# Optimization experiments

Hardware: AMD Instinct MI355X
Metric: run time of the kernel (lower is better)

## Reference

```python
import jax, jax.numpy as jnp
import numpy as np

B, N, C = 8, 4096, 1024
H = 16
D = C // H  # head_dim = 64
SCALE = D ** -0.5


def setup_inputs() -> dict:
    key = jax.random.key(0)
    ks = jax.random.split(key, 5)
    std = C ** -0.5
    return {
        "x": jax.random.normal(ks[0], (B, N, C), dtype=jnp.float32),
        "Wq": jax.random.normal(ks[1], (C, C), dtype=jnp.float32) * std,
        "Wk": jax.random.normal(ks[2], (C, C), dtype=jnp.float32) * std,
        "Wv": jax.random.normal(ks[3], (C, C), dtype=jnp.float32) * std,
        "Wo": jax.random.normal(ks[4], (C, C), dtype=jnp.float32) * std,
        "bo": jnp.zeros((C,), dtype=jnp.float32),
    }


def reference(x, Wq, Wk, Wv, Wo, bo):
    b, n, c = x.shape
    # projections -> (B, N, H, D)
    q = (x @ Wq).reshape(b, n, H, D)
    k = (x @ Wk).reshape(b, n, H, D)
    v = (x @ Wv).reshape(b, n, H, D)
    # feature maps: softmax over head_dim for q, over sequence for k
    q = jax.nn.softmax(q, axis=-1) * SCALE
    k = jax.nn.softmax(k, axis=1)
    # O(N) linear attention: kv summary then apply to q
    kv = jnp.einsum("bnhf,bnhd->bhfd", k, v)   # (B, H, D, D)
    y = jnp.einsum("bnhf,bhfd->bnhd", q, kv)   # (B, N, H, D)
    y = y.reshape(b, n, H * D)
    return y @ Wo + bo
```

## Files before the change

### kernel.cpp

```cpp
#include <hip/hip_runtime.h>


typedef unsigned short u16;
typedef __bf16 bf16x8v __attribute__((ext_vector_type(8)));
typedef float f32x4 __attribute__((ext_vector_type(4)));
typedef u16 u16x8 __attribute__((ext_vector_type(8)));
typedef u16 u16x4 __attribute__((ext_vector_type(4)));

#define AS1C(p) (const __attribute__((address_space(1))) void*)(p)
#define AS3(p)  (__attribute__((address_space(3))) void*)(p)

__device__ __forceinline__ float b2f(u16 u) {
    union { unsigned u; float f; } c; c.u = ((unsigned)u) << 16; return c.f;
}
__device__ __forceinline__ u16 f2b(float f) {
    union { float f; unsigned u; } c; c.f = f;
    unsigned x = c.u + 0x7fffu + ((c.u >> 16) & 1u);
    return (u16)(x >> 16);
}

__global__ void cast_x_kernel(const float* __restrict__ in, u16* __restrict__ out, long n4) {
    long i = (long)blockIdx.x * blockDim.x + threadIdx.x;
    long stride = (long)gridDim.x * blockDim.x;
    for (long j = i; j < n4; j += stride) {
        float4 v = ((const float4*)in)[j];
        u16x4 o = { f2b(v.x), f2b(v.y), f2b(v.z), f2b(v.w) };
        ((u16x4*)out)[j] = o;
    }
}

__global__ void transpose_cast(const float* __restrict__ src, u16* __restrict__ dst) {
    __shared__ float tl[64][65];
    int tx = blockIdx.x & 15, ty = blockIdx.x >> 4;
    int j = threadIdx.x & 63, i0 = threadIdx.x >> 6;
    #pragma unroll
    for (int it = 0; it < 16; ++it) {
        int i = it * 4 + i0;
        tl[i][j] = src[(ty * 64 + i) * 1024 + tx * 64 + j];
    }
    __syncthreads();
    #pragma unroll
    for (int it = 0; it < 16; ++it) {
        int i = it * 4 + i0;
        dst[(tx * 64 + i) * 1024 + ty * 64 + j] = f2b(tl[j][i]);
    }
}

template<int OUTMODE>
__global__ __launch_bounds__(512, 2) void gemm256(
    const u16* __restrict__ A, const u16* __restrict__ Bt,
    void* __restrict__ Cout, const float* __restrict__ bias,
    const int lda, const int ldc, const int ntn, const int nwg)
{
    __shared__ __align__(16) u16 lds[65536];
    const int t = threadIdx.x;
    const int w = t >> 6, lane = t & 63;
    const int l16 = lane & 15, g = lane >> 4;
    const int wr = w >> 2, wc = w & 3;

    const int cpx = nwg >> 3;
    const int bid = blockIdx.x;
    const int swzb = (bid & 7) * cpx + (bid >> 3);
    const int tm = swzb / ntn, tn = swzb - tm * ntn;
    const long row0 = (long)tm << 8, col0 = (long)tn << 8;

    const int r0 = t >> 2;
    const int eo = (((t & 3) ^ ((t >> 3) & 3)) << 3);
    const u16* pa0 = A + (row0 + r0) * (long)lda + eo;
    const u16* pa1 = A + (row0 + 128 + r0) * (long)lda + eo;
    const u16* pb0 = Bt + (col0 + r0) * 1024L + eo;
    const u16* pb1 = Bt + (col0 + 128 + r0) * 1024L + eo;
    const int wB = w << 9;

#define STAGE_A(Tt) { const int _b = ((Tt)&3)*16384; const int _k = ((Tt)&31)*32;        \
    __builtin_amdgcn_global_load_lds(AS1C(pa0 + _k), AS3(lds + _b + wB), 16, 0, 0);      \
    __builtin_amdgcn_global_load_lds(AS1C(pa1 + _k), AS3(lds + _b + 4096 + wB), 16, 0, 0); }
#define STAGE_B(Tt) { const int _b = ((Tt)&3)*16384; const int _k = ((Tt)&31)*32;        \
    __builtin_amdgcn_global_load_lds(AS1C(pb0 + _k), AS3(lds + _b + 8192 + wB), 16, 0, 0);  \
    __builtin_amdgcn_global_load_lds(AS1C(pb1 + _k), AS3(lds + _b + 12288 + wB), 16, 0, 0); }

    STAGE_A(0); STAGE_B(0);
    STAGE_A(1); STAGE_B(1);
    STAGE_A(2); STAGE_B(2);

    f32x4 acc[8][4] = {};
    const int sw = ((g ^ ((l16 >> 1) & 3)) << 3);
    const int arow = wr * 128 + l16;
    const int brow = wc * 64 + l16;

    #pragma unroll 4
    for (int T = 0; T < 32; ++T) {
        const int bufE = (T & 3) * 16384;
        const int Tn = T + 3;
        STAGE_A(Tn);
        asm volatile("s_waitcnt vmcnt(10)" ::: "memory");
        __builtin_amdgcn_s_barrier();
        __builtin_amdgcn_sched_barrier(0);
        bf16x8v bfr[4], afr[4];
        #pragma unroll
        for (int ni = 0; ni < 4; ++ni)
            bfr[ni] = __builtin_bit_cast(bf16x8v,
                *(const u16x8*)&lds[bufE + 8192 + (brow + ni * 16) * 32 + sw]);
        #pragma unroll
        for (int mi = 0; mi < 4; ++mi)
            afr[mi] = __builtin_bit_cast(bf16x8v,
                *(const u16x8*)&lds[bufE + (arow + mi * 16) * 32 + sw]);
        __builtin_amdgcn_s_setprio(1);
        #pragma unroll
        for (int mi = 0; mi < 4; ++mi) {
            #pragma unroll
            for (int ni = 0; ni < 4; ++ni)
                acc[mi][ni] = __builtin_amdgcn_mfma_f32_16x16x32_bf16(
                    afr[mi], bfr[ni], acc[mi][ni], 0, 0, 0);
        }
        __builtin_amdgcn_s_setprio(0);
        STAGE_B(Tn);
        bf16x8v afr2[4];
        #pragma unroll
        for (int mi = 0; mi < 4; ++mi)
            afr2[mi] = __builtin_bit_cast(bf16x8v,
                *(const u16x8*)&lds[bufE + (arow + 64 + mi * 16) * 32 + sw]);
        __builtin_amdgcn_s_setprio(1);
        #pragma unroll
        for (int mi = 0; mi < 4; ++mi) {
            #pragma unroll
            for (int ni = 0; ni < 4; ++ni)
                acc[4 + mi][ni] = __builtin_amdgcn_mfma_f32_16x16x32_bf16(
                    afr2[mi], bfr[ni], acc[4 + mi][ni], 0, 0, 0);
        }
        __builtin_amdgcn_s_setprio(0);
        __builtin_amdgcn_s_barrier();
        __builtin_amdgcn_sched_barrier(0);
    }
    asm volatile("s_waitcnt vmcnt(0)" ::: "memory");
#undef STAGE_A
#undef STAGE_B

    const long crow = row0 + wr * 128 + g * 4;
    const long ccol = col0 + wc * 64 + l16;
    if (OUTMODE == 0) {
        u16* Cb = (u16*)Cout;
        #pragma unroll
        for (int mi = 0; mi < 8; ++mi) {
            #pragma unroll
            for (int ni = 0; ni < 4; ++ni) {
                long base = (crow + mi * 16) * (long)ldc + ccol + ni * 16;
                #pragma unroll
                for (int r = 0; r < 4; ++r)
                    Cb[base + (long)r * ldc] = f2b(acc[mi][ni][r]);
            }
        }
    } else {
        float* Cf = (float*)Cout;
        float bv[4];
        #pragma unroll
        for (int ni = 0; ni < 4; ++ni) bv[ni] = bias[ccol + ni * 16];
        #pragma unroll
        for (int mi = 0; mi < 8; ++mi) {
            #pragma unroll
            for (int ni = 0; ni < 4; ++ni) {
                long base = (crow + mi * 16) * (long)ldc + ccol + ni * 16;
                #pragma unroll
                for (int r = 0; r < 4; ++r)
                    Cf[base + (long)r * ldc] = acc[mi][ni][r] + bv[ni];
            }
        }
    }
}

__global__ __launch_bounds__(256) void kv_partial(const u16* __restrict__ qkv,
                                                  float* __restrict__ kvp,
                                                  float* __restrict__ psum) {
    __shared__ __align__(16) float kf_s[64 * 68];
    __shared__ __align__(16) float v_s[64 * 68];
    const int t = threadIdx.x;
    const int bx = blockIdx.x;
    const int nc = bx & 7, h = (bx >> 3) & 15, b = bx >> 7;
    const int f0 = (t >> 4) << 2;
    const int d0 = (t & 15) << 2;
    const int lr = t >> 3, lc = (t & 7) << 3;
    const long rowbase = (long)b * 4096 + nc * 512;
    const u16* kfg = qkv + (rowbase + lr) * 3072 + 1024 + h * 64 + lc;
    const u16* vg = kfg + 1024;
    float acc[4][4] = {};
    float cs[4] = {};
    for (int n0 = 0; n0 < 512; n0 += 64) {
        long go = (long)n0 * 3072;
        u16x8 kr0 = *(const u16x8*)(kfg + go);
        u16x8 kr1 = *(const u16x8*)(kfg + go + 32L * 3072);
        u16x8 vr0 = *(const u16x8*)(vg + go);
        u16x8 vr1 = *(const u16x8*)(vg + go + 32L * 3072);
        f32x4 ke0a, ke0b, ke1a, ke1b, vv0a, vv0b, vv1a, vv1b;
        #pragma unroll
        for (int j = 0; j < 4; ++j) {
            ke0a[j] = __expf(b2f(kr0[j]));     ke0b[j] = __expf(b2f(kr0[j + 4]));
            ke1a[j] = __expf(b2f(kr1[j]));     ke1b[j] = __expf(b2f(kr1[j + 4]));
            vv0a[j] = b2f(vr0[j]);             vv0b[j] = b2f(vr0[j + 4]);
            vv1a[j] = b2f(vr1[j]);             vv1b[j] = b2f(vr1[j + 4]);
        }
        *(f32x4*)&kf_s[lr * 68 + lc]            = ke0a;
        *(f32x4*)&kf_s[lr * 68 + lc + 4]        = ke0b;
        *(f32x4*)&kf_s[(lr + 32) * 68 + lc]     = ke1a;
        *(f32x4*)&kf_s[(lr + 32) * 68 + lc + 4] = ke1b;
        *(f32x4*)&v_s[lr * 68 + lc]             = vv0a;
        *(f32x4*)&v_s[lr * 68 + lc + 4]         = vv0b;
        *(f32x4*)&v_s[(lr + 32) * 68 + lc]      = vv1a;
        *(f32x4*)&v_s[(lr + 32) * 68 + lc + 4]  = vv1b;
        __syncthreads();
        #pragma unroll 8
        for (int r = 0; r < 64; ++r) {
            f32x4 kf4 = *(const f32x4*)&kf_s[r * 68 + f0];
            f32x4 vf4 = *(const f32x4*)&v_s[r * 68 + d0];
            #pragma unroll
            for (int i = 0; i < 4; ++i) {
                cs[i] += kf4[i];
                #pragma unroll
                for (int jj = 0; jj < 4; ++jj)
                    acc[i][jj] += kf4[i] * vf4[jj];
            }
        }
        __syncthreads();
    }
    float* o = kvp + (long)nc * 524288 + ((long)(b * 16 + h)) * 4096;
    #pragma unroll
    for (int i = 0; i < 4; ++i) {
        #pragma unroll
        for (int jj = 0; jj < 4; ++jj)
            o[(f0 + i) * 64 + d0 + jj] = acc[i][jj];
    }
    if ((t & 15) == 0) {
        float* ps = psum + ((long)nc * 128 + b * 16 + h) * 64 + f0;
        #pragma unroll
        for (int i = 0; i < 4; ++i) ps[i] = cs[i];
    }
}

__global__ void kv_combine_T(const float* __restrict__ kvp, const float* __restrict__ psum,
                             u16* __restrict__ kvTb) {
    __shared__ float tl[64 * 65];
    __shared__ float inv_s[64];
    const int bh = blockIdx.x;
    const int t = threadIdx.x;
    if (t < 64) {
        float s = 0.f;
        #pragma unroll
        for (int nc = 0; nc < 8; ++nc) s += psum[((long)nc * 128 + bh) * 64 + t];
        inv_s[t] = 1.0f / s;
    }
    __syncthreads();
    const float* p = kvp + (long)bh * 4096;
    #pragma unroll
    for (int it = 0; it < 16; ++it) {
        int idx = it * 256 + t;
        float v = 0.f;
        #pragma unroll
        for (int nc = 0; nc < 8; ++nc) v += p[(long)nc * 524288 + idx];
        tl[(idx & 63) * 65 + (idx >> 6)] = v * inv_s[idx >> 6];
    }
    __syncthreads();
    u16* o = kvTb + (long)bh * 4096;
    #pragma unroll
    for (int it = 0; it < 16; ++it) {
        int idx = it * 256 + t;
        o[idx] = f2b(tl[(idx >> 6) * 65 + (idx & 63)]);
    }
}

__global__ __launch_bounds__(256) void apply_mfma(u16* __restrict__ qkv,
                                                  const u16* __restrict__ kvTb) {
    __shared__ __align__(16) u16 Qs[8192];
    const int t = threadIdx.x;
    const int bx = blockIdx.x;
    const int nt = bx & 31, h = (bx >> 5) & 15, b = bx >> 9;
    const long n0 = (long)b * 4096 + (long)nt * 128;
    const int wave = t >> 6, lane = t & 63;
    const int wr = wave >> 1, wc = wave & 1;
    const int l16 = lane & 15, g = lane >> 4;

    const int colg = t & 7;
    const int rloc = t >> 3;
    #pragma unroll
    for (int p = 0; p < 4; ++p) {
        const int row = p * 32 + rloc;
        u16x8 qv = *(const u16x8*)(qkv + (n0 + row) * 3072 + h * 64 + colg * 8);
        float f[8];
        #pragma unroll
        for (int j = 0; j < 8; ++j) f[j] = b2f(qv[j]);
        float m = f[0];
        #pragma unroll
        for (int j = 1; j < 8; ++j) m = fmaxf(m, f[j]);
        m = fmaxf(m, __shfl_xor(m, 1)); m = fmaxf(m, __shfl_xor(m, 2)); m = fmaxf(m, __shfl_xor(m, 4));
        float s = 0.f;
        #pragma unroll
        for (int j = 0; j < 8; ++j) { f[j] = __expf(f[j] - m); s += f[j]; }
        s += __shfl_xor(s, 1); s += __shfl_xor(s, 2); s += __shfl_xor(s, 4);
        const float sc = 0.125f / s;
        u16x8 ov;
        #pragma unroll
        for (int j = 0; j < 8; ++j) ov[j] = f2b(f[j] * sc);
        const int chunk = colg ^ (row & 7);
        *(u16x8*)&Qs[row * 64 + chunk * 8] = ov;
    }
    __syncthreads();

    const u16* kvb = kvTb + ((long)(b * 16 + h) << 12);
    bf16x8v bkv[2][2];
    #pragma unroll
    for (int ni = 0; ni < 2; ++ni) {
        #pragma unroll
        for (int ks = 0; ks < 2; ++ks)
            bkv[ni][ks] = __builtin_bit_cast(bf16x8v,
                *(const u16x8*)(kvb + (wc * 32 + ni * 16 + l16) * 64 + ks * 32 + g * 8));
    }
    bf16x8v aq[4][2];
    #pragma unroll
    for (int mi = 0; mi < 4; ++mi) {
        const int row = wr * 64 + mi * 16 + l16;
        #pragma unroll
        for (int ks = 0; ks < 2; ++ks) {
            const int c16 = (ks * 4 + g) ^ (row & 7);
            aq[mi][ks] = __builtin_bit_cast(bf16x8v,
                *(const u16x8*)&Qs[row * 64 + c16 * 8]);
        }
    }
    f32x4 acc[4][2] = {};
    #pragma unroll
    for (int mi = 0; mi < 4; ++mi) {
        #pragma unroll
        for (int ni = 0; ni < 2; ++ni) {
            acc[mi][ni] = __builtin_amdgcn_mfma_f32_16x16x32_bf16(
                aq[mi][0], bkv[ni][0], acc[mi][ni], 0, 0, 0);
            acc[mi][ni] = __builtin_amdgcn_mfma_f32_16x16x32_bf16(
                aq[mi][1], bkv[ni][1], acc[mi][ni], 0, 0, 0);
        }
    }
    #pragma unroll
    for (int mi = 0; mi < 4; ++mi) {
        #pragma unroll
        for (int ni = 0; ni < 2; ++ni) {
            long row = n0 + wr * 64 + mi * 16 + g * 4;
            int col = h * 64 + wc * 32 + ni * 16 + l16;
            #pragma unroll
            for (int r = 0; r < 4; ++r)
                qkv[(row + r) * 3072 + col] = f2b(acc[mi][ni][r]);
        }
    }
}

extern "C" void kernel_launch(void* const* d_in, const int* in_sizes, int n_in,
                              void* d_out, int out_size, void* d_ws, size_t ws_size,
                              hipStream_t stream) {
    (void)in_sizes; (void)n_in; (void)out_size; (void)ws_size;
    const float* x  = (const float*)d_in[0];
    const float* Wq = (const float*)d_in[1];
    const float* Wk = (const float*)d_in[2];
    const float* Wv = (const float*)d_in[3];
    const float* Wo = (const float*)d_in[4];
    const float* bo = (const float*)d_in[5];

    u16* xb  = (u16*)d_ws;
    u16* wt  = xb + 33554432;
    u16* wot = wt + 3145728;
    u16* qkv = wot + 1048576;
    u16*   kvTb = qkv + 100663296;
    float* kvp  = (float*)xb;
    float* psum = kvp + 4194304;

    cast_x_kernel<<<2048, 256, 0, stream>>>(x, xb, 8388608L);
    transpose_cast<<<256, 256, 0, stream>>>(Wq, wt);
    transpose_cast<<<256, 256, 0, stream>>>(Wk, wt + 1048576);
    transpose_cast<<<256, 256, 0, stream>>>(Wv, wt + 2097152);
    transpose_cast<<<256, 256, 0, stream>>>(Wo, wot);
    gemm256<0><<<1536, 512, 0, stream>>>(xb, wt, (void*)qkv, nullptr, 1024, 3072, 12, 1536);
    kv_partial<<<1024, 256, 0, stream>>>(qkv, kvp, psum);
    kv_combine_T<<<128, 256, 0, stream>>>(kvp, psum, kvTb);
    apply_mfma<<<4096, 256, 0, stream>>>(qkv, kvTb);
    gemm256<1><<<512, 512, 0, stream>>>(qkv, wot, d_out, bo, 3072, 1024, 4, 512);
}
```

Before: 445.0 us.

## Load GEMM B fragments directly from global into registers, bypassing LDS

The B operand of the 256x256 GEMM is no longer staged through shared memory via global_load_lds. Each wave now loads its own B fragments straight into double-buffered registers one k-step ahead, which halves LDS usage and removes the B LDS reads. The cost is that B is reloaded from global/L2 redundantly by the two wave rows (no sharing), and there is more register pressure. Under launch_bounds(512,2) this could cause spills, and the wait counts are retuned to match.

```diff
diff --git a/kernel.cpp b/kernel.cpp
--- a/kernel.cpp
+++ b/kernel.cpp
@@ -52,7 +52,7 @@
     void* __restrict__ Cout, const float* __restrict__ bias,
     const int lda, const int ldc, const int ntn, const int nwg)
 {
-    __shared__ __align__(16) u16 lds[65536];
+    __shared__ __align__(16) u16 lds[32768];
     const int t = threadIdx.x;
     const int w = t >> 6, lane = t & 63;
     const int l16 = lane & 15, g = lane >> 4;
@@ -68,39 +68,37 @@
     const int eo = (((t & 3) ^ ((t >> 3) & 3)) << 3);
     const u16* pa0 = A + (row0 + r0) * (long)lda + eo;
     const u16* pa1 = A + (row0 + 128 + r0) * (long)lda + eo;
-    const u16* pb0 = Bt + (col0 + r0) * 1024L + eo;
-    const u16* pb1 = Bt + (col0 + 128 + r0) * 1024L + eo;
     const int wB = w << 9;
 
-#define STAGE_A(Tt) { const int _b = ((Tt)&3)*16384; const int _k = ((Tt)&31)*32;        \
+    const u16* pbB = Bt + (col0 + wc * 64 + l16) * 1024L + g * 8;
+
+#define STAGE_A(Tt) { const int _b = ((Tt)&3)*8192; const int _k = ((Tt)&31)*32;         \
     __builtin_amdgcn_global_load_lds(AS1C(pa0 + _k), AS3(lds + _b + wB), 16, 0, 0);      \
     __builtin_amdgcn_global_load_lds(AS1C(pa1 + _k), AS3(lds + _b + 4096 + wB), 16, 0, 0); }
-#define STAGE_B(Tt) { const int _b = ((Tt)&3)*16384; const int _k = ((Tt)&31)*32;        \
-    __builtin_amdgcn_global_load_lds(AS1C(pb0 + _k), AS3(lds + _b + 8192 + wB), 16, 0, 0);  \
-    __builtin_amdgcn_global_load_lds(AS1C(pb1 + _k), AS3(lds + _b + 12288 + wB), 16, 0, 0); }
-
-    STAGE_A(0); STAGE_B(0);
-    STAGE_A(1); STAGE_B(1);
-    STAGE_A(2); STAGE_B(2);
+#define LOAD_B(bk, Tt) { const long _kb = (long)(Tt) * 32;                               \
+    breg[bk][0] = *(const u16x8*)(pbB + _kb);                                            \
+    breg[bk][1] = *(const u16x8*)(pbB + 16384 + _kb);                                    \
+    breg[bk][2] = *(const u16x8*)(pbB + 32768 + _kb);                                    \
+    breg[bk][3] = *(const u16x8*)(pbB + 49152 + _kb); }
+
+    u16x8 breg[2][4];
+    STAGE_A(0); STAGE_A(1);
+    LOAD_B(0, 0);
+    STAGE_A(2);
 
     f32x4 acc[8][4] = {};
     const int sw = ((g ^ ((l16 >> 1) & 3)) << 3);
     const int arow = wr * 128 + l16;
-    const int brow = wc * 64 + l16;
 
     #pragma unroll 4
     for (int T = 0; T < 32; ++T) {
-        const int bufE = (T & 3) * 16384;
-        const int Tn = T + 3;
-        STAGE_A(Tn);
-        asm volatile("s_waitcnt vmcnt(10)" ::: "memory");
+        const int bufE = (T & 3) * 8192;
+        LOAD_B((T + 1) & 1, T + 1);
+        STAGE_A(T + 3);
+        asm volatile("s_waitcnt vmcnt(8)" ::: "memory");
         __builtin_amdgcn_s_barrier();
         __builtin_amdgcn_sched_barrier(0);
-        bf16x8v bfr[4], afr[4];
-        #pragma unroll
-        for (int ni = 0; ni < 4; ++ni)
-            bfr[ni] = __builtin_bit_cast(bf16x8v,
-                *(const u16x8*)&lds[bufE + 8192 + (brow + ni * 16) * 32 + sw]);
+        bf16x8v afr[4];
         #pragma unroll
         for (int mi = 0; mi < 4; ++mi)
             afr[mi] = __builtin_bit_cast(bf16x8v,
@@ -111,10 +109,10 @@
             #pragma unroll
             for (int ni = 0; ni < 4; ++ni)
                 acc[mi][ni] = __builtin_amdgcn_mfma_f32_16x16x32_bf16(
-                    afr[mi], bfr[ni], acc[mi][ni], 0, 0, 0);
+                    afr[mi], __builtin_bit_cast(bf16x8v, breg[T & 1][ni]),
+                    acc[mi][ni], 0, 0, 0);
         }
         __builtin_amdgcn_s_setprio(0);
-        STAGE_B(Tn);
         bf16x8v afr2[4];
         #pragma unroll
         for (int mi = 0; mi < 4; ++mi)
@@ -126,7 +124,8 @@
             #pragma unroll
             for (int ni = 0; ni < 4; ++ni)
                 acc[4 + mi][ni] = __builtin_amdgcn_mfma_f32_16x16x32_bf16(
-                    afr2[mi], bfr[ni], acc[4 + mi][ni], 0, 0, 0);
+                    afr2[mi], __builtin_bit_cast(bf16x8v, breg[T & 1][ni]),
+                    acc[4 + mi][ni], 0, 0, 0);
         }
         __builtin_amdgcn_s_setprio(0);
         __builtin_amdgcn_s_barrier();
@@ -134,7 +133,7 @@
     }
     asm volatile("s_waitcnt vmcnt(0)" ::: "memory");
 #undef STAGE_A
-#undef STAGE_B
+#undef LOAD_B
 
     const long crow = row0 + wr * 128 + g * 4;
     const long ccol = col0 + wc * 64 + l16;
```

Measured after the change: 588.6 us. +32.3%, slower.
